# Optimization experiments

Measured on AMD Instinct MI355X. Metric: run time of the kernel, lower is better.

Reference implementation:

```python
import jax, jax.numpy as jnp
import numpy as np

N, F_IN, H, C, D, NH, L, FF = 4096, 256, 2, 64, 128, 4, 2, 2048
DEG = 32


def setup_inputs() -> dict:
    key = jax.random.key(0)
    ks = jax.random.split(key, 32)
    s = 0.05
    # graph: random edges + self loops (PyG GATConv adds self loops)
    src = jax.random.randint(ks[0], (N * DEG,), 0, N)
    dst = jax.random.randint(ks[1], (N * DEG,), 0, N)
    loop = jnp.arange(N)
    edge_index = jnp.stack([jnp.concatenate([src, loop]),
                            jnp.concatenate([dst, loop])]).astype(jnp.int64)
    inp = {
        'x': jax.random.normal(ks[2], (N, F_IN), jnp.float32),
        'edge_index': edge_index,
        'enc_w1': jax.random.normal(ks[3], (F_IN, 128), jnp.float32) * s,
        'enc_b1': jnp.zeros((128,), jnp.float32),
        'enc_w2': jax.random.normal(ks[4], (128, D), jnp.float32) * s,
        'enc_b2': jnp.zeros((D,), jnp.float32),
        'gat_w': jax.random.normal(ks[5], (D, H * C), jnp.float32) * s,
        'gat_asrc': jax.random.normal(ks[6], (H, C), jnp.float32) * s,
        'gat_adst': jax.random.normal(ks[7], (H, C), jnp.float32) * s,
        'gat_bias': jnp.zeros((H * C,), jnp.float32),
        't_wq': jax.random.normal(ks[8], (L, D, D), jnp.float32) * s,
        't_bq': jnp.zeros((L, D), jnp.float32),
        't_wk': jax.random.normal(ks[9], (L, D, D), jnp.float32) * s,
        't_bk': jnp.zeros((L, D), jnp.float32),
        't_wv': jax.random.normal(ks[10], (L, D, D), jnp.float32) * s,
        't_bv': jnp.zeros((L, D), jnp.float32),
        't_wo': jax.random.normal(ks[11], (L, D, D), jnp.float32) * s,
        't_bo': jnp.zeros((L, D), jnp.float32),
        't_ln1_g': jnp.ones((L, D), jnp.float32),
        't_ln1_b': jnp.zeros((L, D), jnp.float32),
        't_ln2_g': jnp.ones((L, D), jnp.float32),
        't_ln2_b': jnp.zeros((L, D), jnp.float32),
        't_w1': jax.random.normal(ks[12], (L, D, FF), jnp.float32) * s,
        't_b1': jnp.zeros((L, FF), jnp.float32),
        't_w2': jax.random.normal(ks[13], (L, FF, D), jnp.float32) * s,
        't_b2': jnp.zeros((L, D), jnp.float32),
    }
    return inp


def _layer_norm(v, g, b):
    m = v.mean(-1, keepdims=True)
    var = v.var(-1, keepdims=True)
    return (v - m) / jnp.sqrt(var + 1e-5) * g + b


def _forward(x, edge_index, enc_w1, enc_b1, enc_w2, enc_b2,
             gat_w, gat_asrc, gat_adst, gat_bias,
             t_wq, t_bq, t_wk, t_bk, t_wv, t_bv, t_wo, t_bo,
             t_ln1_g, t_ln1_b, t_ln2_g, t_ln2_b, t_w1, t_b1, t_w2, t_b2):
    n = x.shape[0]
    # encoder MLP: Linear -> ReLU -> Linear
    h = jnp.maximum(x @ enc_w1 + enc_b1, 0.0) @ enc_w2 + enc_b2  # [N, D]
    # GATConv (concat heads), dropout inactive (eval)
    heads, ch = gat_asrc.shape
    hh = (h @ gat_w).reshape(n, heads, ch)                       # [N, H, C]
    src, dst = edge_index[0], edge_index[1]
    a_src = (hh * gat_asrc).sum(-1)                              # [N, H]
    a_dst = (hh * gat_adst).sum(-1)
    e = jax.nn.leaky_relu(a_src[src] + a_dst[dst], 0.2)          # [E, H]
    # segment softmax over destination nodes
    e_max = jax.ops.segment_max(e, dst, num_segments=n)
    e_exp = jnp.exp(e - e_max[dst])
    denom = jax.ops.segment_sum(e_exp, dst, num_segments=n)
    alpha = e_exp / denom[dst]                                   # [E, H]
    agg = jax.ops.segment_sum(alpha[:, :, None] * hh[src], dst, num_segments=n)
    y = agg.reshape(n, heads * ch) + gat_bias                    # [N, D]
    # TransformerEncoder (post-LN, relu FFN), unbatched sequence of N nodes
    d = y.shape[-1]
    dh = d // NH
    for l in range(t_wq.shape[0]):
        q = (y @ t_wq[l] + t_bq[l]).reshape(n, NH, dh)
        k = (y @ t_wk[l] + t_bk[l]).reshape(n, NH, dh)
        v = (y @ t_wv[l] + t_bv[l]).reshape(n, NH, dh)
        scores = jnp.einsum('nhd,mhd->hnm', q, k) / jnp.sqrt(jnp.float32(dh))
        p = jax.nn.softmax(scores, axis=-1)
        a = jnp.einsum('hnm,mhd->nhd', p, v).reshape(n, d)
        a = a @ t_wo[l] + t_bo[l]
        y = _layer_norm(y + a, t_ln1_g[l], t_ln1_b[l])
        f = jnp.maximum(y @ t_w1[l] + t_b1[l], 0.0) @ t_w2[l] + t_b2[l]
        y = _layer_norm(y + f, t_ln2_g[l], t_ln2_b[l])
    return y


def reference(x, edge_index, enc_w1, enc_b1, enc_w2, enc_b2,
              gat_w, gat_asrc, gat_adst, gat_bias,
              t_wq, t_bq, t_wk, t_bk, t_wv, t_bv, t_wo, t_bo,
              t_ln1_g, t_ln1_b, t_ln2_g, t_ln2_b, t_w1, t_b1, t_w2, t_b2):
    return _forward(x, edge_index, enc_w1, enc_b1, enc_w2, enc_b2,
                    gat_w, gat_asrc, gat_adst, gat_bias,
                    t_wq, t_bq, t_wk, t_bk, t_wv, t_bv, t_wo, t_bo,
                    t_ln1_g, t_ln1_b, t_ln2_g, t_ln2_b, t_w1, t_b1, t_w2, t_b2)
```

## Files before the change

kernel.cpp:

```cpp
#include <hip/hip_runtime.h>

typedef unsigned short u16;
typedef unsigned int u32;
typedef __attribute__((ext_vector_type(8))) short bh8;
typedef __attribute__((ext_vector_type(4))) float fx4;
typedef __attribute__((ext_vector_type(4))) short s4;
typedef __attribute__((ext_vector_type(2))) unsigned int u32x2;

#define QS 0.2550437194342803f

__device__ __forceinline__ u16 f2bf(float f) {
    unsigned u = __float_as_uint(f);
    u += 0x7fffu + ((u >> 16) & 1u);
    return (u16)(u >> 16);
}

__device__ __forceinline__ float bf2f(u16 b) {
    return __uint_as_float((u32)b << 16);
}

__device__ __forceinline__ u32 cvtpk(float lo, float hi) {
    u32 r;
    asm("v_cvt_pk_bf16_f32 %0, %1, %2" : "=v"(r) : "v"(lo), "v"(hi));
    return r;
}

__global__ __launch_bounds__(256) void prep_kernel(
    const float* x, const float* ew1, const float* ew2, const float* gw,
    const float* wq, const float* wk, const float* wv, const float* wo,
    const float* w1, const float* w2,
    const float* bq, const float* bk, const float* bv,
    u16* xb, u16* ew1t, u16* ew2t, u16* gwt,
    u16* wqkvt, float* bqkv, u16* wot, u16* w1t, u16* w2t)
{
    __shared__ u16 tile[64 * 65];
    int bid = blockIdx.x;
    const int t = threadIdx.x;

    if (bid < 128) {
        const float4* x4 = (const float4*)x;
        s4* o4 = (s4*)xb;
        #pragma unroll
        for (int i = 0; i < 8; i++) {
            int fi = bid * 2048 + i * 256 + t;
            float4 v = x4[fi];
            s4 o = { (short)f2bf(v.x), (short)f2bf(v.y), (short)f2bf(v.z), (short)f2bf(v.w) };
            o4[fi] = o;
        }
        return;
    }
    bid -= 128;
    if (bid < 1) {
        for (int idx = t; idx < 768; idx += 256) {
            int l = idx / 384, n = idx % 384;
            float v;
            if (n < 128)      v = bq[l * 128 + n] * QS;
            else if (n < 256) v = bk[l * 128 + n - 128];
            else              v = bv[l * 128 + n - 256];
            bqkv[idx] = v;
        }
        return;
    }
    bid -= 1;

    const float* src; u16* dst; int R, C, tr, tc; float sc = 1.f;
    if (bid < 8)            { src = ew1; dst = ew1t; R = 256; C = 128; tr = bid >> 1; tc = bid & 1; }
    else if ((bid -= 8) < 4)  { src = ew2; dst = ew2t; R = 128; C = 128; tr = bid >> 1; tc = bid & 1; }
    else if ((bid -= 4) < 4)  { src = gw;  dst = gwt;  R = 128; C = 128; tr = bid >> 1; tc = bid & 1; }
    else if ((bid -= 4) < 24) {
        int l = bid / 12, r2 = bid % 12, which = r2 >> 2, i = r2 & 3;
        R = 128; C = 128; tr = i >> 1; tc = i & 1;
        if (which == 0)      { src = wq + l * 16384; dst = wqkvt + l * 49152;         sc = QS; }
        else if (which == 1) { src = wk + l * 16384; dst = wqkvt + l * 49152 + 16384; }
        else                 { src = wv + l * 16384; dst = wqkvt + l * 49152 + 32768; }
    }
    else if ((bid -= 24) < 8)   { int l = bid >> 2, i = bid & 3;  src = wo + l * 16384; dst = wot + l * 16384; R = 128; C = 128; tr = i >> 1; tc = i & 1; }
    else if ((bid -= 8) < 128)  { int l = bid >> 6, i = bid & 63; src = w1 + (size_t)l * 262144; dst = w1t + (size_t)l * 262144; R = 128;  C = 2048; tr = i & 1;  tc = i >> 1; }
    else { bid -= 128;            int l = bid >> 6, i = bid & 63; src = w2 + (size_t)l * 262144; dst = w2t + (size_t)l * 262144; R = 2048; C = 128;  tr = i >> 1; tc = i & 1; }

    const int r = t >> 2, cs = (t & 3) * 16;
    const float* sp = src + (size_t)(tr * 64 + r) * C + tc * 64 + cs;
    #pragma unroll
    for (int j = 0; j < 16; j++) tile[r * 65 + cs + j] = f2bf(sp[j] * sc);
    __syncthreads();
    u16* dp = dst + (size_t)(tc * 64 + r) * R + tr * 64 + cs;
    #pragma unroll
    for (int j = 0; j < 16; j++) dp[j] = tile[(cs + j) * 65 + r];
}

__global__ __launch_bounds__(256) void gemm_bf16(
    const u16* __restrict__ A, const u16* __restrict__ Bt,
    const float* __restrict__ bias,
    float* __restrict__ Cf, u16* __restrict__ Cb, float* __restrict__ Cpart,
    u16* __restrict__ Cvt,
    int M, int N, int K, int relu, int kchunk, int ldc)
{
    __shared__ __align__(16) u16 As[2][64][40];
    __shared__ __align__(16) u16 Bs[2][64][40];
    const int m0 = blockIdx.x * 64, n0 = blockIdx.y * 64, z = blockIdx.z;
    const int tid = threadIdx.x;
    const int lane = tid & 63, w = tid >> 6;
    const int wm = (w >> 1) * 32, wn = (w & 1) * 32;
    const int l15 = lane & 15, l4 = lane >> 4;
    const int srow = tid >> 2, skq = (tid & 3) * 8;
    const int k0 = z * kchunk;

    const u16* Ap = A + (size_t)(m0 + srow) * K + k0 + skq;
    const u16* Bp = Bt + (size_t)(n0 + srow) * K + k0 + skq;

    fx4 acc00 = {0,0,0,0}, acc01 = {0,0,0,0}, acc10 = {0,0,0,0}, acc11 = {0,0,0,0};

    *(int4*)&As[0][srow][skq] = *(const int4*)Ap;
    *(int4*)&Bs[0][srow][skq] = *(const int4*)Bp;

    const int niter = kchunk >> 5;
    for (int it = 0; it < niter; it++) {
        const int cur = it & 1;
        int4 ar, br;
        __syncthreads();
        if (it + 1 < niter) {
            ar = *(const int4*)(Ap + (it + 1) * 32);
            br = *(const int4*)(Bp + (it + 1) * 32);
        }
        bh8 a0 = *(const bh8*)&As[cur][wm + l15][l4 * 8];
        bh8 a1 = *(const bh8*)&As[cur][wm + 16 + l15][l4 * 8];
        bh8 b0 = *(const bh8*)&Bs[cur][wn + l15][l4 * 8];
        bh8 b1 = *(const bh8*)&Bs[cur][wn + 16 + l15][l4 * 8];
        acc00 = __builtin_amdgcn_mfma_f32_16x16x32_bf16(a0, b0, acc00, 0, 0, 0);
        acc01 = __builtin_amdgcn_mfma_f32_16x16x32_bf16(a0, b1, acc01, 0, 0, 0);
        acc10 = __builtin_amdgcn_mfma_f32_16x16x32_bf16(a1, b0, acc10, 0, 0, 0);
        acc11 = __builtin_amdgcn_mfma_f32_16x16x32_bf16(a1, b1, acc11, 0, 0, 0);
        if (it + 1 < niter) {
            *(int4*)&As[cur ^ 1][srow][skq] = ar;
            *(int4*)&Bs[cur ^ 1][srow][skq] = br;
        }
    }

    fx4* accs[2][2] = {{&acc00, &acc01}, {&acc10, &acc11}};
    #pragma unroll
    for (int i = 0; i < 2; i++)
        #pragma unroll
        for (int j = 0; j < 2; j++) {
            int colg = n0 + wn + j * 16 + l15;
            int rowb = m0 + wm + i * 16 + l4 * 4;
            if (Cpart) {
                float* cp = Cpart + (size_t)z * M * N;
                #pragma unroll
                for (int r = 0; r < 4; r++)
                    cp[(size_t)(rowb + r) * N + colg] = (*accs[i][j])[r];
                continue;
            }
            float bvv = bias ? bias[colg] : 0.f;
            float vals[4];
            #pragma unroll
            for (int r = 0; r < 4; r++) {
                float v = (*accs[i][j])[r] + bvv;
                vals[r] = relu ? fmaxf(v, 0.f) : v;
            }
            if (Cvt && colg >= 256) {
                s4 pk = { (short)f2bf(vals[0]), (short)f2bf(vals[1]),
                          (short)f2bf(vals[2]), (short)f2bf(vals[3]) };
                *(s4*)&Cvt[(size_t)(colg - 256) * 4096 + rowb] = pk;
            } else {
                #pragma unroll
                for (int r = 0; r < 4; r++) {
                    if (Cf) Cf[(size_t)(rowb + r) * ldc + colg] = vals[r];
                    if (Cb) Cb[(size_t)(rowb + r) * ldc + colg] = f2bf(vals[r]);
                }
            }
        }
}

__global__ __launch_bounds__(256) void encoder_gat(
    const u16* __restrict__ xb, const u16* __restrict__ ew1t,
    const float* __restrict__ eb1,
    const u16* __restrict__ ew2t, const float* __restrict__ eb2,
    const u16* __restrict__ gwt,
    const float* __restrict__ gasrc, const float* __restrict__ gadst,
    u16* __restrict__ hhb, float* __restrict__ ansrc,
    float* __restrict__ andst, int* __restrict__ counts)
{
    __shared__ __align__(16) u16 As[32][264];
    __shared__ __align__(16) u16 Bs[2][128][40];
    __shared__ __align__(16) u16 Hb[32][136];
    __shared__ float Ct[32][132];
    const int m0 = blockIdx.x * 32;
    const int tid = threadIdx.x;
    const int lane = tid & 63, w = tid >> 6;
    const int wm = (w >> 1) * 16, wn = (w & 1) * 64;
    const int l15 = lane & 15, l4 = lane >> 4;

    if (tid < 32) counts[blockIdx.x * 32 + tid] = 0;

    {
        const int row = tid >> 3, c0 = (tid & 7) * 32;
        const u16* ap = xb + (size_t)(m0 + row) * 256 + c0;
        #pragma unroll
        for (int i = 0; i < 4; i++)
            *(int4*)&As[row][c0 + i * 8] = *(const int4*)(ap + i * 8);
    }
    {
        #pragma unroll
        for (int i = 0; i < 2; i++) {
            int s = tid + i * 256, r = s >> 2, c = (s & 3) * 8;
            *(int4*)&Bs[0][r][c] = *(const int4*)&ew1t[(size_t)r * 256 + c];
        }
    }

    fx4 acc[4] = {};
    for (int it = 0; it < 8; it++) {
        const int cur = it & 1;
        int4 br[2];
        __syncthreads();
        if (it < 7) {
            #pragma unroll
            for (int i = 0; i < 2; i++) {
                int s = tid + i * 256, r = s >> 2, c = (s & 3) * 8;
                br[i] = *(const int4*)&ew1t[(size_t)r * 256 + (it + 1) * 32 + c];
            }
        }
        bh8 af = *(const bh8*)&As[wm + l15][it * 32 + l4 * 8];
        #pragma unroll
        for (int nj = 0; nj < 4; nj++) {
            bh8 bf = *(const bh8*)&Bs[cur][wn + nj * 16 + l15][l4 * 8];
            acc[nj] = __builtin_amdgcn_mfma_f32_16x16x32_bf16(af, bf, acc[nj], 0, 0, 0);
        }
        if (it < 7) {
            #pragma unroll
            for (int i = 0; i < 2; i++) {
                int s = tid + i * 256, r = s >> 2, c = (s & 3) * 8;
                *(int4*)&Bs[cur ^ 1][r][c] = br[i];
            }
        }
    }
    #pragma unroll
    for (int nj = 0; nj < 4; nj++) {
        int cl = wn + nj * 16 + l15;
        float bvv = eb1[cl];
        #pragma unroll
        for (int r = 0; r < 4; r++)
            Hb[wm + l4 * 4 + r][cl] = f2bf(fmaxf(acc[nj][r] + bvv, 0.f));
    }
    {
        #pragma unroll
        for (int i = 0; i < 2; i++) {
            int s = tid + i * 256, r = s >> 2, c = (s & 3) * 8;
            *(int4*)&Bs[0][r][c] = *(const int4*)&ew2t[(size_t)r * 128 + c];
        }
    }

    fx4 acc2[4] = {};
    for (int it = 0; it < 4; it++) {
        const int cur = it & 1;
        int4 br[2];
        __syncthreads();
        if (it < 3) {
            #pragma unroll
            for (int i = 0; i < 2; i++) {
                int s = tid + i * 256, r = s >> 2, c = (s & 3) * 8;
                br[i] = *(const int4*)&ew2t[(size_t)r * 128 + (it + 1) * 32 + c];
            }
        }
        bh8 af = *(const bh8*)&Hb[wm + l15][it * 32 + l4 * 8];
        #pragma unroll
        for (int nj = 0; nj < 4; nj++) {
            bh8 bf = *(const bh8*)&Bs[cur][wn + nj * 16 + l15][l4 * 8];
            acc2[nj] = __builtin_amdgcn_mfma_f32_16x16x32_bf16(af, bf, acc2[nj], 0, 0, 0);
        }
        if (it < 3) {
            #pragma unroll
            for (int i = 0; i < 2; i++) {
                int s = tid + i * 256, r = s >> 2, c = (s & 3) * 8;
                *(int4*)&Bs[cur ^ 1][r][c] = br[i];
            }
        }
    }
    u16 (*Hb2)[136] = (u16(*)[136])&As[0][0];
    #pragma unroll
    for (int nj = 0; nj < 4; nj++) {
        int cl = wn + nj * 16 + l15;
        float bvv = eb2[cl];
        #pragma unroll
        for (int r = 0; r < 4; r++)
            Hb2[wm + l4 * 4 + r][cl] = f2bf(acc2[nj][r] + bvv);
    }
    {
        #pragma unroll
        for (int i = 0; i < 2; i++) {
            int s = tid + i * 256, r = s >> 2, c = (s & 3) * 8;
            *(int4*)&Bs[0][r][c] = *(const int4*)&gwt[(size_t)r * 128 + c];
        }
    }

    fx4 acc3[4] = {};
    for (int it = 0; it < 4; it++) {
        const int cur = it & 1;
        int4 br[2];
        __syncthreads();
        if (it < 3) {
            #pragma unroll
            for (int i = 0; i < 2; i++) {
                int s = tid + i * 256, r = s >> 2, c = (s & 3) * 8;
                br[i] = *(const int4*)&gwt[(size_t)r * 128 + (it + 1) * 32 + c];
            }
        }
        bh8 af = *(const bh8*)&Hb2[wm + l15][it * 32 + l4 * 8];
        #pragma unroll
        for (int nj = 0; nj < 4; nj++) {
            bh8 bf = *(const bh8*)&Bs[cur][wn + nj * 16 + l15][l4 * 8];
            acc3[nj] = __builtin_amdgcn_mfma_f32_16x16x32_bf16(af, bf, acc3[nj], 0, 0, 0);
        }
        if (it < 3) {
            #pragma unroll
            for (int i = 0; i < 2; i++) {
                int s = tid + i * 256, r = s >> 2, c = (s & 3) * 8;
                *(int4*)&Bs[cur ^ 1][r][c] = br[i];
            }
        }
    }

    #pragma unroll
    for (int nj = 0; nj < 4; nj++) {
        int cl = wn + nj * 16 + l15;
        #pragma unroll
        for (int r = 0; r < 4; r++) {
            int rl = wm + l4 * 4 + r;
            float v = acc3[nj][r];
            hhb[(size_t)(m0 + rl) * 128 + cl] = f2bf(v);
            Ct[rl][cl] = v;
        }
    }
    __syncthreads();

    const int row = tid >> 3, c0 = (tid & 7) * 16, head = c0 >> 6;
    float ps = 0.f, pd = 0.f;
    #pragma unroll
    for (int j = 0; j < 16; j++) {
        float v = Ct[row][c0 + j];
        int cc = (c0 + j) & 63;
        ps += v * gasrc[head * 64 + cc];
        pd += v * gadst[head * 64 + cc];
    }
    ps += __shfl_xor(ps, 1); pd += __shfl_xor(pd, 1);
    ps += __shfl_xor(ps, 2); pd += __shfl_xor(pd, 2);
    if ((tid & 3) == 0) {
        ansrc[(m0 + row) * 2 + head] = ps;
        andst[(m0 + row) * 2 + head] = pd;
    }
}

__global__ __launch_bounds__(256) void ffn_fused(
    const u16* __restrict__ A, const u16* __restrict__ W1t,
    const float* __restrict__ b1, const u16* __restrict__ W2t,
    float* __restrict__ part)
{
    __shared__ __align__(16) u16 Ab[64][136];
    __shared__ __align__(16) u16 Wb[64][136];
    __shared__ __align__(16) u16 Sb[64][72];
    const int m0 = blockIdx.x * 64, z = blockIdx.y;
    const int tid = threadIdx.x;
    const int lane = tid & 63, w = tid >> 6;
    const int wm = (w >> 1) * 32;
    const int wn = (w & 1) * 32;
    const int wn2 = (w & 1) * 64;
    const int l15 = lane & 15, l4 = lane >> 4;
    const int sr = tid >> 2, sc = (tid & 3) * 32;

    {
        const u16* ap = A + (size_t)(m0 + sr) * 128 + sc;
        #pragma unroll
        for (int i = 0; i < 4; i++)
            *(int4*)&Ab[sr][sc + i * 8] = *(const int4*)(ap + i * 8);
    }

    fx4 acc2[2][4] = {};

    for (int chunk = 0; chunk < 4; chunk++) {
        const int ffbase = z * 256 + chunk * 64;
        __syncthreads();
        {
            const u16* wp = W1t + (size_t)(ffbase + sr) * 128 + sc;
            #pragma unroll
            for (int i = 0; i < 4; i++)
                *(int4*)&Wb[sr][sc + i * 8] = *(const int4*)(wp + i * 8);
        }
        __syncthreads();

        fx4 s[2][2] = {};
        #pragma unroll
        for (int ks = 0; ks < 4; ks++) {
            bh8 af0 = *(const bh8*)&Ab[wm + l15][ks * 32 + l4 * 8];
            bh8 af1 = *(const bh8*)&Ab[wm + 16 + l15][ks * 32 + l4 * 8];
            bh8 bf0 = *(const bh8*)&Wb[wn + l15][ks * 32 + l4 * 8];
            bh8 bf1 = *(const bh8*)&Wb[wn + 16 + l15][ks * 32 + l4 * 8];
            s[0][0] = __builtin_amdgcn_mfma_f32_16x16x32_bf16(af0, bf0, s[0][0], 0, 0, 0);
            s[0][1] = __builtin_amdgcn_mfma_f32_16x16x32_bf16(af0, bf1, s[0][1], 0, 0, 0);
            s[1][0] = __builtin_amdgcn_mfma_f32_16x16x32_bf16(af1, bf0, s[1][0], 0, 0, 0);
            s[1][1] = __builtin_amdgcn_mfma_f32_16x16x32_bf16(af1, bf1, s[1][1], 0, 0, 0);
        }
        #pragma unroll
        for (int mi = 0; mi < 2; mi++)
            #pragma unroll
            for (int nj = 0; nj < 2; nj++) {
                float bv = b1[ffbase + wn + nj * 16 + l15];
                #pragma unroll
                for (int r = 0; r < 4; r++) {
                    float v = fmaxf(s[mi][nj][r] + bv, 0.f);
                    Sb[wm + mi * 16 + l4 * 4 + r][wn + nj * 16 + l15] = f2bf(v);
                }
            }
        __syncthreads();

        #pragma unroll
        for (int ks = 0; ks < 2; ks++) {
            bh8 af0 = *(const bh8*)&Sb[wm + l15][ks * 32 + l4 * 8];
            bh8 af1 = *(const bh8*)&Sb[wm + 16 + l15][ks * 32 + l4 * 8];
            #pragma unroll
            for (int nj = 0; nj < 4; nj++) {
                bh8 bf = *(const bh8*)&W2t[(size_t)(wn2 + nj * 16 + l15) * 2048 + ffbase + ks * 32 + l4 * 8];
                acc2[0][nj] = __builtin_amdgcn_mfma_f32_16x16x32_bf16(af0, bf, acc2[0][nj], 0, 0, 0);
                acc2[1][nj] = __builtin_amdgcn_mfma_f32_16x16x32_bf16(af1, bf, acc2[1][nj], 0, 0, 0);
            }
        }
    }

    float* cp = part + (size_t)z * 524288;
    #pragma unroll
    for (int mi = 0; mi < 2; mi++)
        #pragma unroll
        for (int nj = 0; nj < 4; nj++) {
            int colg = wn2 + nj * 16 + l15;
            int rowb = m0 + wm + mi * 16 + l4 * 4;
            #pragma unroll
            for (int r = 0; r < 4; r++)
                cp[(size_t)(rowb + r) * 128 + colg] = acc2[mi][nj][r];
        }
}

__global__ void count_edges(const int* __restrict__ dst, int* counts, int E) {
    int i = blockIdx.x * 256 + threadIdx.x;
    if (i < E) atomicAdd(&counts[dst[i]], 1);
}

__global__ __launch_bounds__(1024) void scan_kernel(const int* __restrict__ counts,
                                                    int* row_start, int* cursor) {
    __shared__ int wsum[16];
    int tid = threadIdx.x, lane = tid & 63, wv = tid >> 6;
    int b = tid * 4;
    int c0 = counts[b], c1 = counts[b+1], c2 = counts[b+2], c3 = counts[b+3];
    int sum = c0 + c1 + c2 + c3;
    int inc = sum;
    #pragma unroll
    for (int off = 1; off < 64; off <<= 1) {
        int v = __shfl_up(inc, off);
        if (lane >= off) inc += v;
    }
    if (lane == 63) wsum[wv] = inc;
    __syncthreads();
    int base = 0;
    #pragma unroll
    for (int i = 0; i < 16; i++) {
        int v = wsum[i];
        base += (i < wv) ? v : 0;
    }
    int excl = base + inc - sum;
    int r0 = excl, r1 = excl + c0, r2 = r1 + c1, r3 = r2 + c2;
    row_start[b] = r0; row_start[b+1] = r1; row_start[b+2] = r2; row_start[b+3] = r3;
    cursor[b] = r0; cursor[b+1] = r1; cursor[b+2] = r2; cursor[b+3] = r3;
    if (tid == 1023) row_start[4096] = base + inc;
}

__global__ void scatter_edges(const int* __restrict__ src, const int* __restrict__ dst,
                              int* cursor, int* csr_src, int E) {
    int i = blockIdx.x * 256 + threadIdx.x;
    if (i < E) { int pos = atomicAdd(&cursor[dst[i]], 1); csr_src[pos] = src[i]; }
}

__global__ __launch_bounds__(256) void gat_aggregate(
    const int* __restrict__ row_start, const int* __restrict__ csr_src,
    const float* __restrict__ an_src, const float* __restrict__ an_dst,
    const u16* __restrict__ hhb, const float* __restrict__ gbias,
    float* __restrict__ y32, u16* __restrict__ yb)
{
    int n = blockIdx.x, tid = threadIdx.x;
    const int lane = tid & 63, wv = tid >> 6;
    int start = row_start[n], end = row_start[n + 1];
    float ad0 = an_dst[n * 2 + 0], ad1 = an_dst[n * 2 + 1];
    __shared__ float rmx[4][2], rsm[4][2];
    __shared__ float sal0[128], sal1[128], sagg[256];
    __shared__ int sidx[128];

    float mx0 = -1e30f, mx1 = -1e30f;
    for (int i = start + tid; i < end; i += 256) {
        int s = csr_src[i];
        float e0 = an_src[s * 2 + 0] + ad0; e0 = e0 > 0.f ? e0 : 0.2f * e0;
        float e1 = an_src[s * 2 + 1] + ad1; e1 = e1 > 0.f ? e1 : 0.2f * e1;
        mx0 = fmaxf(mx0, e0); mx1 = fmaxf(mx1, e1);
    }
    for (int off = 32; off; off >>= 1) { mx0 = fmaxf(mx0, __shfl_down(mx0, off)); mx1 = fmaxf(mx1, __shfl_down(mx1, off)); }
    if (lane == 0) { rmx[wv][0] = mx0; rmx[wv][1] = mx1; }
    __syncthreads();
    mx0 = fmaxf(fmaxf(rmx[0][0], rmx[1][0]), fmaxf(rmx[2][0], rmx[3][0]));
    mx1 = fmaxf(fmaxf(rmx[0][1], rmx[1][1]), fmaxf(rmx[2][1], rmx[3][1]));

    float den0 = 0.f, den1 = 0.f;
    for (int i = start + tid; i < end; i += 256) {
        int s = csr_src[i];
        float e0 = an_src[s * 2 + 0] + ad0; e0 = e0 > 0.f ? e0 : 0.2f * e0;
        float e1 = an_src[s * 2 + 1] + ad1; e1 = e1 > 0.f ? e1 : 0.2f * e1;
        den0 += __expf(e0 - mx0); den1 += __expf(e1 - mx1);
    }
    for (int off = 32; off; off >>= 1) { den0 += __shfl_down(den0, off); den1 += __shfl_down(den1, off); }
    if (lane == 0) { rsm[wv][0] = den0; rsm[wv][1] = den1; }
    __syncthreads();
    den0 = rsm[0][0] + rsm[1][0] + rsm[2][0] + rsm[3][0];
    den1 = rsm[0][1] + rsm[1][1] + rsm[2][1] + rsm[3][1];
    float rd0 = 1.f / den0, rd1 = 1.f / den1;

    const int grp = tid >> 7, ch = tid & 127, head = ch >> 6;
    float agg = 0.f;
    for (int c0 = start; c0 < end; c0 += 128) {
        int cnt = min(128, end - c0);
        __syncthreads();
        if (tid < cnt) {
            int s = csr_src[c0 + tid];
            float e0 = an_src[s * 2 + 0] + ad0; e0 = e0 > 0.f ? e0 : 0.2f * e0;
            float e1 = an_src[s * 2 + 1] + ad1; e1 = e1 > 0.f ? e1 : 0.2f * e1;
            sal0[tid] = __expf(e0 - mx0) * rd0;
            sal1[tid] = __expf(e1 - mx1) * rd1;
            sidx[tid] = s;
        }
        __syncthreads();
        const float* sal = head ? sal1 : sal0;
        for (int j = grp; j < cnt; j += 2)
            agg += sal[j] * bf2f(hhb[(size_t)sidx[j] * 128 + ch]);
    }
    sagg[tid] = agg;
    __syncthreads();
    if (tid < 128) {
        float v = sagg[tid] + sagg[tid + 128] + gbias[tid];
        y32[(size_t)n * 128 + tid] = v;
        yb[(size_t)n * 128 + tid] = f2bf(v);
    }
}

__global__ __launch_bounds__(256) void flash_attn_part(
    const u16* __restrict__ q, const u16* __restrict__ k,
    const u16* __restrict__ vt, float* __restrict__ po,
    float* __restrict__ pm, float* __restrict__ pl)
{
    __shared__ __align__(16) u16 Kb[2][64][40];
    __shared__ __align__(16) u16 Vb[2][32][72];
    __shared__ __align__(16) u16 Ps[4][16][72];
    const int q0 = blockIdx.x * 64, h = blockIdx.y, ch = blockIdx.z;
    const int tid = threadIdx.x;
    const int w = tid >> 6, lane = tid & 63, l15 = lane & 15, l4 = lane >> 4;

    bh8 qf = *(const bh8*)&q[(size_t)(q0 + w * 16 + l15) * 256 + h * 32 + l4 * 8];

    const int skey = tid >> 2, sds = (tid & 3) * 8;
    const int svd = tid >> 3, svk = (tid & 7) * 8;
    const u16* kgp = &k[(size_t)(ch * 1024 + skey) * 256 + h * 32 + sds];
    const u16* vgp = &vt[(size_t)(h * 32 + svd) * 4096 + ch * 1024 + svk];

    fx4 o0 = {0,0,0,0}, o1 = {0,0,0,0};
    float M = -1e30f, L = 0.f;

    *(int4*)&Kb[0][skey][sds] = *(const int4*)kgp;
    *(int4*)&Vb[0][svd][svk] = *(const int4*)vgp;

    for (int ti = 0; ti < 16; ti++) {
        const int cur = ti & 1;
        int4 kr, vr;
        __syncthreads();
        if (ti < 15) {
            kr = *(const int4*)(kgp + (size_t)(ti + 1) * 64 * 256);
            vr = *(const int4*)(vgp + (ti + 1) * 64);
        }

        fx4 s[4];
        #pragma unroll
        for (int sub = 0; sub < 4; sub++) {
            bh8 kf = *(const bh8*)&Kb[cur][sub * 16 + l15][l4 * 8];
            fx4 z = {0,0,0,0};
            s[sub] = __builtin_amdgcn_mfma_f32_16x16x32_bf16(kf, qf, z, 0, 0, 0);
        }
        float t0 = fmaxf(fmaxf(s[0][0], s[0][1]), s[0][2]);
        float t1 = fmaxf(fmaxf(s[0][3], s[1][0]), s[1][1]);
        float t2 = fmaxf(fmaxf(s[1][2], s[1][3]), s[2][0]);
        float t3 = fmaxf(fmaxf(s[2][1], s[2][2]), s[2][3]);
        float t4 = fmaxf(fmaxf(s[3][0], s[3][1]), s[3][2]);
        float pmax = fmaxf(fmaxf(fmaxf(t0, t1), t2), fmaxf(fmaxf(t3, t4), s[3][3]));
        pmax = fmaxf(pmax, __shfl_xor(pmax, 16));
        pmax = fmaxf(pmax, __shfl_xor(pmax, 32));
        if (!__all(pmax - M <= 8.0f)) {
            float f = __builtin_amdgcn_exp2f(M - pmax);
            M = pmax;
            o0 *= f; o1 *= f; L *= f;
        }

        #pragma unroll
        for (int sub = 0; sub < 4; sub++)
            #pragma unroll
            for (int r = 0; r < 4; r++)
                s[sub][r] = __builtin_amdgcn_exp2f(s[sub][r] - M);
        float ss0 = (s[0][0] + s[0][1]) + (s[0][2] + s[0][3]);
        float ss1 = (s[1][0] + s[1][1]) + (s[1][2] + s[1][3]);
        float ss2 = (s[2][0] + s[2][1]) + (s[2][2] + s[2][3]);
        float ss3 = (s[3][0] + s[3][1]) + (s[3][2] + s[3][3]);
        float lsum = (ss0 + ss1) + (ss2 + ss3);
        lsum += __shfl_xor(lsum, 16);
        lsum += __shfl_xor(lsum, 32);
        L += lsum;

        #pragma unroll
        for (int sub = 0; sub < 4; sub++) {
            u32x2 pk = { cvtpk(s[sub][0], s[sub][1]), cvtpk(s[sub][2], s[sub][3]) };
            *(u32x2*)&Ps[w][l15][sub * 16 + l4 * 4] = pk;
        }

        #pragma unroll
        for (int kc = 0; kc < 2; kc++) {
            bh8 bf  = *(const bh8*)&Ps[w][l15][kc * 32 + l4 * 8];
            bh8 af0 = *(const bh8*)&Vb[cur][l15][kc * 32 + l4 * 8];
            bh8 af1 = *(const bh8*)&Vb[cur][16 + l15][kc * 32 + l4 * 8];
            o0 = __builtin_amdgcn_mfma_f32_16x16x32_bf16(af0, bf, o0, 0, 0, 0);
            o1 = __builtin_amdgcn_mfma_f32_16x16x32_bf16(af1, bf, o1, 0, 0, 0);
        }

        if (ti < 15) {
            *(int4*)&Kb[cur ^ 1][skey][sds] = kr;
            *(int4*)&Vb[cur ^ 1][svd][svk] = vr;
        }
    }
    const int base = (blockIdx.x * 4 + h) * 4 + ch;
    const int qrow = w * 16 + l15;
    *(fx4*)&po[(size_t)(base * 64 + qrow) * 32 + l4 * 4]      = o0;
    *(fx4*)&po[(size_t)(base * 64 + qrow) * 32 + 16 + l4 * 4] = o1;
    if (l4 == 0) { pm[base * 64 + qrow] = M; pl[base * 64 + qrow] = L; }
}

__global__ __launch_bounds__(256) void oproj_cln(
    const float* __restrict__ po, const float* __restrict__ pm,
    const float* __restrict__ pl, const u16* __restrict__ Bt,
    const float* __restrict__ bias, const float* __restrict__ g,
    const float* __restrict__ b,
    float* __restrict__ y32, u16* __restrict__ yb)
{
    __shared__ __align__(16) u16 Ab[32][136];
    __shared__ __align__(16) u16 Bs[2][128][40];
    __shared__ float Ct[32][132];
    const int m0 = blockIdx.x * 32;
    const int tid = threadIdx.x;
    const int lane = tid & 63, w = tid >> 6;
    const int wm = (w >> 1) * 16, wn = (w & 1) * 64;
    const int l15 = lane & 15, l4 = lane >> 4;

    {
        const int row = tid >> 3, c0 = (tid & 7) * 16;
        const int gr = m0 + row, qb = gr >> 6, r64 = gr & 63, h = c0 >> 5;
        const int rb = (qb * 4 + h) * 4;
        float mv0 = pm[(rb + 0) * 64 + r64], mv1 = pm[(rb + 1) * 64 + r64];
        float mv2 = pm[(rb + 2) * 64 + r64], mv3 = pm[(rb + 3) * 64 + r64];
        float ms = fmaxf(fmaxf(mv0, mv1), fmaxf(mv2, mv3));
        float wc[4];
        wc[0] = __builtin_amdgcn_exp2f(mv0 - ms);
        wc[1] = __builtin_amdgcn_exp2f(mv1 - ms);
        wc[2] = __builtin_amdgcn_exp2f(mv2 - ms);
        wc[3] = __builtin_amdgcn_exp2f(mv3 - ms);
        float lsum = wc[0] * pl[(rb + 0) * 64 + r64] + wc[1] * pl[(rb + 1) * 64 + r64]
                   + wc[2] * pl[(rb + 2) * 64 + r64] + wc[3] * pl[(rb + 3) * 64 + r64];
        float rl = 1.f / lsum;
        const int cb = c0 & 31;
        float o[16] = {};
        #pragma unroll
        for (int c = 0; c < 4; c++) {
            const float* pp = po + ((size_t)((rb + c) * 64 + r64)) * 32 + cb;
            #pragma unroll
            for (int jj = 0; jj < 4; jj++) {
                fx4 v = *(const fx4*)(pp + jj * 4);
                o[jj * 4 + 0] += wc[c] * v[0];
                o[jj * 4 + 1] += wc[c] * v[1];
                o[jj * 4 + 2] += wc[c] * v[2];
                o[jj * 4 + 3] += wc[c] * v[3];
            }
        }
        #pragma unroll
        for (int j = 0; j < 16; j++)
            Ab[row][c0 + j] = f2bf(o[j] * rl);
    }

    {
        const int brow = tid >> 2, bkq = (tid & 3) * 8;
        *(int4*)&Bs[0][brow][bkq]      = *(const int4*)&Bt[(size_t)brow * 128 + bkq];
        *(int4*)&Bs[0][brow + 64][bkq] = *(const int4*)&Bt[(size_t)(brow + 64) * 128 + bkq];
    }

    fx4 acc[4] = {};
    const int brow = tid >> 2, bkq = (tid & 3) * 8;
    for (int it = 0; it < 4; it++) {
        const int cur = it & 1;
        int4 br0, br1;
        __syncthreads();
        if (it < 3) {
            br0 = *(const int4*)&Bt[(size_t)brow * 128 + (it + 1) * 32 + bkq];
            br1 = *(const int4*)&Bt[(size_t)(brow + 64) * 128 + (it + 1) * 32 + bkq];
        }
        bh8 af = *(const bh8*)&Ab[wm + l15][it * 32 + l4 * 8];
        #pragma unroll
        for (int nj = 0; nj < 4; nj++) {
            bh8 bf = *(const bh8*)&Bs[cur][wn + nj * 16 + l15][l4 * 8];
            acc[nj] = __builtin_amdgcn_mfma_f32_16x16x32_bf16(af, bf, acc[nj], 0, 0, 0);
        }
        if (it < 3) {
            *(int4*)&Bs[cur ^ 1][brow][bkq]      = br0;
            *(int4*)&Bs[cur ^ 1][brow + 64][bkq] = br1;
        }
    }

    #pragma unroll
    for (int nj = 0; nj < 4; nj++) {
        int cl = wn + nj * 16 + l15;
        float bvv = bias[cl];
        #pragma unroll
        for (int r = 0; r < 4; r++) {
            int rl = wm + l4 * 4 + r;
            Ct[rl][cl] = acc[nj][r] + bvv + y32[(size_t)(m0 + rl) * 128 + cl];
        }
    }
    __syncthreads();

    const int row = tid >> 3, c0 = (tid & 7) * 16;
    float s1 = 0.f, s2 = 0.f;
    #pragma unroll
    for (int j = 0; j < 16; j++) { float v = Ct[row][c0 + j]; s1 += v; s2 += v * v; }
    #pragma unroll
    for (int off = 1; off < 8; off <<= 1) { s1 += __shfl_xor(s1, off); s2 += __shfl_xor(s2, off); }
    float mean = s1 * (1.f / 128.f);
    float var = s2 * (1.f / 128.f) - mean * mean;
    float rstd = rsqrtf(var + 1e-5f);
    #pragma unroll
    for (int j = 0; j < 16; j++) {
        int col = c0 + j;
        float o = (Ct[row][col] - mean) * rstd * g[col] + b[col];
        y32[(size_t)(m0 + row) * 128 + col] = o;
        yb[(size_t)(m0 + row) * 128 + col] = f2bf(o);
    }
}

__global__ __launch_bounds__(128) void add_ln_p(
    const float* __restrict__ y, const float* __restrict__ part, int nz,
    const float* __restrict__ bias,
    const float* __restrict__ g, const float* __restrict__ b,
    float* __restrict__ out32, u16* __restrict__ outb)
{
    int n = blockIdx.x, tid = threadIdx.x;
    float v = y[(size_t)n * 128 + tid] + bias[tid];
    for (int z = 0; z < nz; z++) v += part[(size_t)z * 524288 + n * 128 + tid];
    float sacc = v;
    for (int off = 32; off; off >>= 1) sacc += __shfl_down(sacc, off);
    __shared__ float sm[2], sv[2];
    if ((tid & 63) == 0) sm[tid >> 6] = sacc;
    __syncthreads();
    float mean = (sm[0] + sm[1]) * (1.f / 128.f);
    float d = v - mean;
    float qacc = d * d;
    for (int off = 32; off; off >>= 1) qacc += __shfl_down(qacc, off);
    if ((tid & 63) == 0) sv[tid >> 6] = qacc;
    __syncthreads();
    float var = (sv[0] + sv[1]) * (1.f / 128.f);
    float o = d * rsqrtf(var + 1e-5f) * g[tid] + b[tid];
    out32[(size_t)n * 128 + tid] = o;
    outb[(size_t)n * 128 + tid] = f2bf(o);
}

extern "C" void kernel_launch(void* const* d_in, const int* in_sizes, int n_in,
                              void* d_out, int out_size, void* d_ws, size_t ws_size,
                              hipStream_t stream)
{
    const float* x     = (const float*)d_in[0];
    const int*   ei    = (const int*)  d_in[1];
    const float* ew1   = (const float*)d_in[2];
    const float* eb1   = (const float*)d_in[3];
    const float* ew2   = (const float*)d_in[4];
    const float* eb2   = (const float*)d_in[5];
    const float* gw    = (const float*)d_in[6];
    const float* gasrc = (const float*)d_in[7];
    const float* gadst = (const float*)d_in[8];
    const float* gbias = (const float*)d_in[9];
    const float* wq    = (const float*)d_in[10];
    const float* bq    = (const float*)d_in[11];
    const float* wk    = (const float*)d_in[12];
    const float* bk    = (const float*)d_in[13];
    const float* wv    = (const float*)d_in[14];
    const float* bv    = (const float*)d_in[15];
    const float* wo    = (const float*)d_in[16];
    const float* bo    = (const float*)d_in[17];
    const float* ln1g  = (const float*)d_in[18];
    const float* ln1b  = (const float*)d_in[19];
    const float* ln2g  = (const float*)d_in[20];
    const float* ln2b  = (const float*)d_in[21];
    const float* w1    = (const float*)d_in[22];
    const float* b1    = (const float*)d_in[23];
    const float* w2    = (const float*)d_in[24];
    const float* b2    = (const float*)d_in[25];

    const int E = in_sizes[1] / 2;
    const int* esrc = ei;
    const int* edst = ei + E;

    char* p = (char*)d_ws;
    auto alloc = [&](size_t bytes) -> void* {
        void* r = (void*)p;
        p += (bytes + 255) & ~(size_t)255;
        return r;
    };
    u16* xb    = (u16*)alloc(4096 * 256 * 2);
    u16* ew1t  = (u16*)alloc(128 * 256 * 2);
    u16* ew2t  = (u16*)alloc(128 * 128 * 2);
    u16* gwt   = (u16*)alloc(128 * 128 * 2);
    u16* wqkvt = (u16*)alloc(2 * 384 * 128 * 2);
    float* bqkv = (float*)alloc(2 * 384 * 4);
    u16* wot   = (u16*)alloc(2 * 128 * 128 * 2);
    u16* w1t   = (u16*)alloc(2 * 2048 * 128 * 2);
    u16* w2t   = (u16*)alloc(2 * 128 * 2048 * 2);
    u16* hhb   = (u16*)alloc(4096 * 128 * 2);
    float* ansrc = (float*)alloc(4096 * 2 * 4);
    float* andst = (float*)alloc(4096 * 2 * 4);
    int* counts    = (int*)alloc(4096 * 4);
    int* row_start = (int*)alloc(4097 * 4);
    int* cursor    = (int*)alloc(4096 * 4);
    int* csr_src   = (int*)alloc((size_t)E * 4);
    float* y32 = (float*)alloc(4096 * 128 * 4);
    u16* yb    = (u16*)alloc(4096 * 128 * 2);
    u16* qkvb  = (u16*)alloc((size_t)4096 * 256 * 2);
    u16* vtb   = (u16*)alloc(4096 * 128 * 2);
    float* po  = (float*)alloc((size_t)64 * 4 * 4 * 64 * 32 * 4);
    float* pm  = (float*)alloc(64 * 4 * 4 * 64 * 4);
    float* pl  = (float*)alloc(64 * 4 * 4 * 64 * 4);
    float* ffpart = (float*)alloc((size_t)8 * 4096 * 128 * 4);

    prep_kernel<<<433, 256, 0, stream>>>(x, ew1, ew2, gw, wq, wk, wv, wo, w1, w2,
                                         bq, bk, bv,
                                         xb, ew1t, ew2t, gwt, wqkvt, bqkv, wot, w1t, w2t);

    encoder_gat<<<128, 256, 0, stream>>>(xb, ew1t, eb1, ew2t, eb2, gwt,
                                         gasrc, gadst, hhb, ansrc, andst, counts);
    count_edges<<<(E + 255) / 256, 256, 0, stream>>>(edst, counts, E);
    scan_kernel<<<1, 1024, 0, stream>>>(counts, row_start, cursor);
    scatter_edges<<<(E + 255) / 256, 256, 0, stream>>>(esrc, edst, cursor, csr_src, E);
    gat_aggregate<<<4096, 256, 0, stream>>>(row_start, csr_src, ansrc, andst, hhb, gbias, y32, yb);

    for (int l = 0; l < 2; l++) {
        gemm_bf16<<<dim3(64, 6), 256, 0, stream>>>(yb, wqkvt + l * 49152, bqkv + l * 384, nullptr, qkvb, nullptr, vtb, 4096, 384, 128, 0, 128, 256);
        flash_attn_part<<<dim3(64, 4, 4), 256, 0, stream>>>(qkvb, qkvb + 128, vtb, po, pm, pl);
        oproj_cln<<<128, 256, 0, stream>>>(po, pm, pl, wot + l * 16384, bo + l * 128, ln1g + l * 128, ln1b + l * 128, y32, yb);
        ffn_fused<<<dim3(64, 8), 256, 0, stream>>>(yb, w1t + (size_t)l * 262144, b1 + l * 2048, w2t + (size_t)l * 262144, ffpart);
        float* outp = (l == 1) ? (float*)d_out : y32;
        add_ln_p<<<4096, 128, 0, stream>>>(y32, ffpart, 8, b2 + l * 128, ln2g + l * 128, ln2b + l * 128, outp, yb);
    }
}
```

Measured before the change: 181.1 us.

## Process 32 query rows per wave in flash attention, split keys 8 ways

```diff
diff --git a/kernel.cpp b/kernel.cpp
--- a/kernel.cpp
+++ b/kernel.cpp
@@ -551,93 +551,134 @@
 {
     __shared__ __align__(16) u16 Kb[2][64][40];
     __shared__ __align__(16) u16 Vb[2][32][72];
-    __shared__ __align__(16) u16 Ps[4][16][72];
-    const int q0 = blockIdx.x * 64, h = blockIdx.y, ch = blockIdx.z;
+    __shared__ __align__(16) u16 Ps[4][32][72];
+    const int q0 = blockIdx.x * 128, h = blockIdx.y, ch = blockIdx.z;
     const int tid = threadIdx.x;
     const int w = tid >> 6, lane = tid & 63, l15 = lane & 15, l4 = lane >> 4;
 
-    bh8 qf = *(const bh8*)&q[(size_t)(q0 + w * 16 + l15) * 256 + h * 32 + l4 * 8];
+    bh8 qf0 = *(const bh8*)&q[(size_t)(q0 + w * 32 + l15) * 256 + h * 32 + l4 * 8];
+    bh8 qf1 = *(const bh8*)&q[(size_t)(q0 + w * 32 + 16 + l15) * 256 + h * 32 + l4 * 8];
 
     const int skey = tid >> 2, sds = (tid & 3) * 8;
     const int svd = tid >> 3, svk = (tid & 7) * 8;
-    const u16* kgp = &k[(size_t)(ch * 1024 + skey) * 256 + h * 32 + sds];
-    const u16* vgp = &vt[(size_t)(h * 32 + svd) * 4096 + ch * 1024 + svk];
-
-    fx4 o0 = {0,0,0,0}, o1 = {0,0,0,0};
-    float M = -1e30f, L = 0.f;
+    const u16* kgp = &k[(size_t)(ch * 512 + skey) * 256 + h * 32 + sds];
+    const u16* vgp = &vt[(size_t)(h * 32 + svd) * 4096 + ch * 512 + svk];
+
+    fx4 o00 = {0,0,0,0}, o01 = {0,0,0,0}, o10 = {0,0,0,0}, o11 = {0,0,0,0};
+    float M0 = -1e30f, L0 = 0.f, M1 = -1e30f, L1 = 0.f;
 
     *(int4*)&Kb[0][skey][sds] = *(const int4*)kgp;
     *(int4*)&Vb[0][svd][svk] = *(const int4*)vgp;
 
-    for (int ti = 0; ti < 16; ti++) {
+    for (int ti = 0; ti < 8; ti++) {
         const int cur = ti & 1;
         int4 kr, vr;
         __syncthreads();
-        if (ti < 15) {
+        if (ti < 7) {
             kr = *(const int4*)(kgp + (size_t)(ti + 1) * 64 * 256);
             vr = *(const int4*)(vgp + (ti + 1) * 64);
         }
 
-        fx4 s[4];
+        fx4 s0[4], s1[4];
         #pragma unroll
         for (int sub = 0; sub < 4; sub++) {
             bh8 kf = *(const bh8*)&Kb[cur][sub * 16 + l15][l4 * 8];
             fx4 z = {0,0,0,0};
-            s[sub] = __builtin_amdgcn_mfma_f32_16x16x32_bf16(kf, qf, z, 0, 0, 0);
-        }
-        float t0 = fmaxf(fmaxf(s[0][0], s[0][1]), s[0][2]);
-        float t1 = fmaxf(fmaxf(s[0][3], s[1][0]), s[1][1]);
-        float t2 = fmaxf(fmaxf(s[1][2], s[1][3]), s[2][0]);
-        float t3 = fmaxf(fmaxf(s[2][1], s[2][2]), s[2][3]);
-        float t4 = fmaxf(fmaxf(s[3][0], s[3][1]), s[3][2]);
-        float pmax = fmaxf(fmaxf(fmaxf(t0, t1), t2), fmaxf(fmaxf(t3, t4), s[3][3]));
-        pmax = fmaxf(pmax, __shfl_xor(pmax, 16));
-        pmax = fmaxf(pmax, __shfl_xor(pmax, 32));
-        if (!__all(pmax - M <= 8.0f)) {
-            float f = __builtin_amdgcn_exp2f(M - pmax);
-            M = pmax;
-            o0 *= f; o1 *= f; L *= f;
-        }
-
-        #pragma unroll
-        for (int sub = 0; sub < 4; sub++)
-            #pragma unroll
-            for (int r = 0; r < 4; r++)
-                s[sub][r] = __builtin_amdgcn_exp2f(s[sub][r] - M);
-        float ss0 = (s[0][0] + s[0][1]) + (s[0][2] + s[0][3]);
-        float ss1 = (s[1][0] + s[1][1]) + (s[1][2] + s[1][3]);
-        float ss2 = (s[2][0] + s[2][1]) + (s[2][2] + s[2][3]);
-        float ss3 = (s[3][0] + s[3][1]) + (s[3][2] + s[3][3]);
-        float lsum = (ss0 + ss1) + (ss2 + ss3);
-        lsum += __shfl_xor(lsum, 16);
-        lsum += __shfl_xor(lsum, 32);
-        L += lsum;
+            s0[sub] = __builtin_amdgcn_mfma_f32_16x16x32_bf16(kf, qf0, z, 0, 0, 0);
+            s1[sub] = __builtin_amdgcn_mfma_f32_16x16x32_bf16(kf, qf1, z, 0, 0, 0);
+        }
+        {
+            float t0 = fmaxf(fmaxf(s0[0][0], s0[0][1]), s0[0][2]);
+            float t1 = fmaxf(fmaxf(s0[0][3], s0[1][0]), s0[1][1]);
+            float t2 = fmaxf(fmaxf(s0[1][2], s0[1][3]), s0[2][0]);
+            float t3 = fmaxf(fmaxf(s0[2][1], s0[2][2]), s0[2][3]);
+            float t4 = fmaxf(fmaxf(s0[3][0], s0[3][1]), s0[3][2]);
+            float pmax = fmaxf(fmaxf(fmaxf(t0, t1), t2), fmaxf(fmaxf(t3, t4), s0[3][3]));
+            pmax = fmaxf(pmax, __shfl_xor(pmax, 16));
+            pmax = fmaxf(pmax, __shfl_xor(pmax, 32));
+            if (!__all(pmax - M0 <= 8.0f)) {
+                float f = __builtin_amdgcn_exp2f(M0 - pmax);
+                M0 = pmax;
+                o00 *= f; o01 *= f; L0 *= f;
+            }
+            #pragma unroll
+            for (int sub = 0; sub < 4; sub++)
+                #pragma unroll
+                for (int r = 0; r < 4; r++)
+                    s0[sub][r] = __builtin_amdgcn_exp2f(s0[sub][r] - M0);
+            float ss0 = (s0[0][0] + s0[0][1]) + (s0[0][2] + s0[0][3]);
+            float ss1 = (s0[1][0] + s0[1][1]) + (s0[1][2] + s0[1][3]);
+            float ss2 = (s0[2][0] + s0[2][1]) + (s0[2][2] + s0[2][3]);
+            float ss3 = (s0[3][0] + s0[3][1]) + (s0[3][2] + s0[3][3]);
+            float lsum = (ss0 + ss1) + (ss2 + ss3);
+            lsum += __shfl_xor(lsum, 16);
+            lsum += __shfl_xor(lsum, 32);
+            L0 += lsum;
+        }
+        {
+            float t0 = fmaxf(fmaxf(s1[0][0], s1[0][1]), s1[0][2]);
+            float t1 = fmaxf(fmaxf(s1[0][3], s1[1][0]), s1[1][1]);
+            float t2 = fmaxf(fmaxf(s1[1][2], s1[1][3]), s1[2][0]);
+            float t3 = fmaxf(fmaxf(s1[2][1], s1[2][2]), s1[2][3]);
+            float t4 = fmaxf(fmaxf(s1[3][0], s1[3][1]), s1[3][2]);
+            float pmax = fmaxf(fmaxf(fmaxf(t0, t1), t2), fmaxf(fmaxf(t3, t4), s1[3][3]));
+            pmax = fmaxf(pmax, __shfl_xor(pmax, 16));
+            pmax = fmaxf(pmax, __shfl_xor(pmax, 32));
+            if (!__all(pmax - M1 <= 8.0f)) {
+                float f = __builtin_amdgcn_exp2f(M1 - pmax);
+                M1 = pmax;
+                o10 *= f; o11 *= f; L1 *= f;
+            }
+            #pragma unroll
+            for (int sub = 0; sub < 4; sub++)
+                #pragma unroll
+                for (int r = 0; r < 4; r++)
+                    s1[sub][r] = __builtin_amdgcn_exp2f(s1[sub][r] - M1);
+            float ss0 = (s1[0][0] + s1[0][1]) + (s1[0][2] + s1[0][3]);
+            float ss1 = (s1[1][0] + s1[1][1]) + (s1[1][2] + s1[1][3]);
+            float ss2 = (s1[2][0] + s1[2][1]) + (s1[2][2] + s1[2][3]);
+            float ss3 = (s1[3][0] + s1[3][1]) + (s1[3][2] + s1[3][3]);
+            float lsum = (ss0 + ss1) + (ss2 + ss3);
+            lsum += __shfl_xor(lsum, 16);
+            lsum += __shfl_xor(lsum, 32);
+            L1 += lsum;
+        }
 
         #pragma unroll
         for (int sub = 0; sub < 4; sub++) {
-            u32x2 pk = { cvtpk(s[sub][0], s[sub][1]), cvtpk(s[sub][2], s[sub][3]) };
-            *(u32x2*)&Ps[w][l15][sub * 16 + l4 * 4] = pk;
+            u32x2 pk0 = { cvtpk(s0[sub][0], s0[sub][1]), cvtpk(s0[sub][2], s0[sub][3]) };
+            *(u32x2*)&Ps[w][l15][sub * 16 + l4 * 4] = pk0;
+            u32x2 pk1 = { cvtpk(s1[sub][0], s1[sub][1]), cvtpk(s1[sub][2], s1[sub][3]) };
+            *(u32x2*)&Ps[w][16 + l15][sub * 16 + l4 * 4] = pk1;
         }
 
         #pragma unroll
         for (int kc = 0; kc < 2; kc++) {
-            bh8 bf  = *(const bh8*)&Ps[w][l15][kc * 32 + l4 * 8];
+            bh8 bfA = *(const bh8*)&Ps[w][l15][kc * 32 + l4 * 8];
+            bh8 bfB = *(const bh8*)&Ps[w][16 + l15][kc * 32 + l4 * 8];
             bh8 af0 = *(const bh8*)&Vb[cur][l15][kc * 32 + l4 * 8];
             bh8 af1 = *(const bh8*)&Vb[cur][16 + l15][kc * 32 + l4 * 8];
-            o0 = __builtin_amdgcn_mfma_f32_16x16x32_bf16(af0, bf, o0, 0, 0, 0);
-            o1 = __builtin_amdgcn_mfma_f32_16x16x32_bf16(af1, bf, o1, 0, 0, 0);
-        }
-
-        if (ti < 15) {
+            o00 = __builtin_amdgcn_mfma_f32_16x16x32_bf16(af0, bfA, o00, 0, 0, 0);
+            o01 = __builtin_amdgcn_mfma_f32_16x16x32_bf16(af1, bfA, o01, 0, 0, 0);
+            o10 = __builtin_amdgcn_mfma_f32_16x16x32_bf16(af0, bfB, o10, 0, 0, 0);
+            o11 = __builtin_amdgcn_mfma_f32_16x16x32_bf16(af1, bfB, o11, 0, 0, 0);
+        }
+
+        if (ti < 7) {
             *(int4*)&Kb[cur ^ 1][skey][sds] = kr;
             *(int4*)&Vb[cur ^ 1][svd][svk] = vr;
         }
     }
-    const int base = (blockIdx.x * 4 + h) * 4 + ch;
-    const int qrow = w * 16 + l15;
-    *(fx4*)&po[(size_t)(base * 64 + qrow) * 32 + l4 * 4]      = o0;
-    *(fx4*)&po[(size_t)(base * 64 + qrow) * 32 + 16 + l4 * 4] = o1;
-    if (l4 == 0) { pm[base * 64 + qrow] = M; pl[base * 64 + qrow] = L; }
+    const int base = (blockIdx.x * 4 + h) * 8 + ch;
+    const int qA = w * 32 + l15, qB = qA + 16;
+    *(fx4*)&po[(size_t)(base * 128 + qA) * 32 + l4 * 4]      = o00;
+    *(fx4*)&po[(size_t)(base * 128 + qA) * 32 + 16 + l4 * 4] = o01;
+    *(fx4*)&po[(size_t)(base * 128 + qB) * 32 + l4 * 4]      = o10;
+    *(fx4*)&po[(size_t)(base * 128 + qB) * 32 + 16 + l4 * 4] = o11;
+    if (l4 == 0) {
+        pm[base * 128 + qA] = M0; pl[base * 128 + qA] = L0;
+        pm[base * 128 + qB] = M1; pl[base * 128 + qB] = L1;
+    }
 }
 
 __global__ __launch_bounds__(256) void oproj_cln(
@@ -658,24 +699,24 @@
 
     {
         const int row = tid >> 3, c0 = (tid & 7) * 16;
-        const int gr = m0 + row, qb = gr >> 6, r64 = gr & 63, h = c0 >> 5;
-        const int rb = (qb * 4 + h) * 4;
-        float mv0 = pm[(rb + 0) * 64 + r64], mv1 = pm[(rb + 1) * 64 + r64];
-        float mv2 = pm[(rb + 2) * 64 + r64], mv3 = pm[(rb + 3) * 64 + r64];
-        float ms = fmaxf(fmaxf(mv0, mv1), fmaxf(mv2, mv3));
-        float wc[4];
-        wc[0] = __builtin_amdgcn_exp2f(mv0 - ms);
-        wc[1] = __builtin_amdgcn_exp2f(mv1 - ms);
-        wc[2] = __builtin_amdgcn_exp2f(mv2 - ms);
-        wc[3] = __builtin_amdgcn_exp2f(mv3 - ms);
-        float lsum = wc[0] * pl[(rb + 0) * 64 + r64] + wc[1] * pl[(rb + 1) * 64 + r64]
-                   + wc[2] * pl[(rb + 2) * 64 + r64] + wc[3] * pl[(rb + 3) * 64 + r64];
+        const int gr = m0 + row, qb = gr >> 7, r1 = gr & 127, h = c0 >> 5;
+        const int rb = (qb * 4 + h) * 8;
+        float ms = -1e30f;
+        float mv[8];
+        #pragma unroll
+        for (int c = 0; c < 8; c++) { mv[c] = pm[(rb + c) * 128 + r1]; ms = fmaxf(ms, mv[c]); }
+        float wc[8], lsum = 0.f;
+        #pragma unroll
+        for (int c = 0; c < 8; c++) {
+            wc[c] = __builtin_amdgcn_exp2f(mv[c] - ms);
+            lsum += wc[c] * pl[(rb + c) * 128 + r1];
+        }
         float rl = 1.f / lsum;
         const int cb = c0 & 31;
         float o[16] = {};
         #pragma unroll
-        for (int c = 0; c < 4; c++) {
-            const float* pp = po + ((size_t)((rb + c) * 64 + r64)) * 32 + cb;
+        for (int c = 0; c < 8; c++) {
+            const float* pp = po + ((size_t)((rb + c) * 128 + r1)) * 32 + cb;
             #pragma unroll
             for (int jj = 0; jj < 4; jj++) {
                 fx4 v = *(const fx4*)(pp + jj * 4);
@@ -835,9 +876,9 @@
     u16* yb    = (u16*)alloc(4096 * 128 * 2);
     u16* qkvb  = (u16*)alloc((size_t)4096 * 256 * 2);
     u16* vtb   = (u16*)alloc(4096 * 128 * 2);
-    float* po  = (float*)alloc((size_t)64 * 4 * 4 * 64 * 32 * 4);
-    float* pm  = (float*)alloc(64 * 4 * 4 * 64 * 4);
-    float* pl  = (float*)alloc(64 * 4 * 4 * 64 * 4);
+    float* po  = (float*)alloc((size_t)32 * 4 * 8 * 128 * 32 * 4);
+    float* pm  = (float*)alloc(32 * 4 * 8 * 128 * 4);
+    float* pl  = (float*)alloc(32 * 4 * 8 * 128 * 4);
     float* ffpart = (float*)alloc((size_t)8 * 4096 * 128 * 4);
 
     prep_kernel<<<433, 256, 0, stream>>>(x, ew1, ew2, gw, wq, wk, wv, wo, w1, w2,
@@ -853,7 +894,7 @@
 
     for (int l = 0; l < 2; l++) {
         gemm_bf16<<<dim3(64, 6), 256, 0, stream>>>(yb, wqkvt + l * 49152, bqkv + l * 384, nullptr, qkvb, nullptr, vtb, 4096, 384, 128, 0, 128, 256);
-        flash_attn_part<<<dim3(64, 4, 4), 256, 0, stream>>>(qkvb, qkvb + 128, vtb, po, pm, pl);
+        flash_attn_part<<<dim3(32, 4, 8), 256, 0, stream>>>(qkvb, qkvb + 128, vtb, po, pm, pl);
         oproj_cln<<<128, 256, 0, stream>>>(po, pm, pl, wot + l * 16384, bo + l * 128, ln1g + l * 128, ln1b + l * 128, y32, yb);
         ffn_fused<<<dim3(64, 8), 256, 0, stream>>>(yb, w1t + (size_t)l * 262144, b1 + l * 2048, w2t + (size_t)l * 262144, ffpart);
         float* outp = (l == 1) ? (float*)d_out : y32;
```

New measurement: 180.1 us. About the same (-0.6%).
